# Performance work log

Hardware: AMD Instinct MI355X
Metric: run time of the kernel (lower is better)

## Reference

```python
import jax, jax.numpy as jnp
import numpy as np

HOPS = 2
BN_EPS = 1e-5


def _glorot(key, shape):
    fan_in = shape[-2]
    bound = 1.0 / np.sqrt(fan_in)
    return jax.random.uniform(key, shape, jnp.float32, -bound, bound)


def setup_inputs() -> dict:
    key = jax.random.key(0)
    ks = jax.random.split(key, 12)
    n, e = 50000, 800000
    in_c, hid, out_c = 128, 96, 64
    x = jax.random.normal(ks[0], (n, in_c), jnp.float32)
    edge_index = jax.random.randint(ks[1], (2, e), 0, n, jnp.int32)
    # MixHopLayer 0: hops+1 linears in_c -> hid (stacked)
    conv0_W = _glorot(ks[2], (HOPS + 1, in_c, hid))
    conv0_b = jnp.zeros((HOPS + 1, hid), jnp.float32)
    # MixHopLayer 1: hops+1 linears hid*(hops+1) -> out_c
    conv1_W = _glorot(ks[3], (HOPS + 1, hid * (HOPS + 1), out_c))
    conv1_b = jnp.zeros((HOPS + 1, out_c), jnp.float32)
    # BatchNorm1d(hid*(hops+1)) eval-mode params/buffers
    w = hid * (HOPS + 1)
    bn_gamma = jnp.ones((w,), jnp.float32)
    bn_beta = jnp.zeros((w,), jnp.float32)
    bn_mean = 0.1 * jax.random.normal(ks[4], (w,), jnp.float32)
    bn_var = jnp.ones((w,), jnp.float32) + 0.1 * jax.random.uniform(ks[5], (w,))
    # final projection out_c*(hops+1) -> out_c
    fp_W = _glorot(ks[6], (out_c * (HOPS + 1), out_c))
    fp_b = jnp.zeros((out_c,), jnp.float32)
    return dict(x=x, edge_index=edge_index, conv0_W=conv0_W, conv0_b=conv0_b,
                conv1_W=conv1_W, conv1_b=conv1_b, bn_gamma=bn_gamma, bn_beta=bn_beta,
                bn_mean=bn_mean, bn_var=bn_var, fp_W=fp_W, fp_b=fp_b)


def _gcn_norm(edge_index, n):
    # PyG gcn_norm with add_self_loops=True, improved=False, symmetric norm.
    row, col = edge_index[0], edge_index[1]
    loop = jnp.arange(n, dtype=edge_index.dtype)
    row = jnp.concatenate([row, loop])
    col = jnp.concatenate([col, loop])
    deg = jax.ops.segment_sum(jnp.ones_like(col, jnp.float32), col, num_segments=n)
    dinv = jnp.where(deg > 0, jax.lax.rsqrt(deg), 0.0)
    w = dinv[row] * dinv[col]
    return row, col, w


def _spmm_adj_t(row, col, w, x, n):
    # adj_t = SparseTensor(row=col, col=row, value=w): out[col] += w * x[row]
    return jax.ops.segment_sum(w[:, None] * x[row], col, num_segments=n)


def _mixhop_layer(x, W, b, row, col, w, n):
    xs = [x @ W[0] + b[0]]
    for j in range(1, HOPS + 1):
        xj = x @ W[j] + b[j]
        for _ in range(j):
            xj = _spmm_adj_t(row, col, w, xj, n)
        xs.append(xj)
    return jnp.concatenate(xs, axis=1)


def reference(x, edge_index, conv0_W, conv0_b, conv1_W, conv1_b,
              bn_gamma, bn_beta, bn_mean, bn_var, fp_W, fp_b):
    n = x.shape[0]
    row, col, w = _gcn_norm(edge_index, n)
    h = _mixhop_layer(x, conv0_W, conv0_b, row, col, w, n)
    # BatchNorm1d (eval) + ReLU; dropout is identity in eval
    h = bn_gamma * (h - bn_mean) * jax.lax.rsqrt(bn_var + BN_EPS) + bn_beta
    h = jax.nn.relu(h)
    h = _mixhop_layer(h, conv1_W, conv1_b, row, col, w, n)
    return h @ fp_W + fp_b
```

## Files before the change

kernel.cpp:

```cpp
#include <hip/hip_runtime.h>

#define IN_C 128
#define HID 96
#define OUT_C 64
#define W0C 288
#define W1C 192
#define CAP 5120
#define EPB 1024

typedef __bf16 bf16x8v __attribute__((ext_vector_type(8)));
typedef float  f32x4v  __attribute__((ext_vector_type(4)));


__global__ void k_combo_prep(const float* __restrict__ x, __bf16* __restrict__ xb, int n8,
                             const float* __restrict__ W0, const float* __restrict__ W1,
                             const float* __restrict__ Wf,
                             const float* __restrict__ gamma, const float* __restrict__ beta,
                             const float* __restrict__ mean, const float* __restrict__ var,
                             __bf16* __restrict__ w0t, __bf16* __restrict__ w1t,
                             __bf16* __restrict__ wft,
                             float* __restrict__ scale, float* __restrict__ shift,
                             int* __restrict__ zp, int nz,
                             int CB, int PB) {
    int b = blockIdx.x;
    if (b < CB) {
        int i = b * 256 + threadIdx.x;
        if (i >= n8) return;
        bf16x8v o;
#pragma unroll
        for (int q = 0; q < 8; q++) o[q] = (__bf16)x[i * 8 + q];
        *(bf16x8v*)(xb + (size_t)i * 8) = o;
    } else if (b < CB + PB) {
        const int T0 = 3 * IN_C * HID;
        const int T1 = 3 * W0C * OUT_C;
        const int T2 = W1C * OUT_C;
        int i = (b - CB) * 256 + threadIdx.x;
        if (i < T0) {
            int kn = IN_C * HID;
            int j = i / kn, r = i % kn;
            int k = r / HID, nn = r % HID;
            w0t[(size_t)j * kn + (size_t)nn * IN_C + k] = (__bf16)W0[i];
        } else if (i < T0 + T1) {
            int ii = i - T0;
            int kn = W0C * OUT_C;
            int j = ii / kn, r = ii % kn;
            int k = r / OUT_C, nn = r % OUT_C;
            w1t[(size_t)j * kn + (size_t)nn * W0C + k] = (__bf16)W1[ii];
        } else if (i < T0 + T1 + T2) {
            int ii = i - T0 - T1;
            int k = ii / OUT_C, nn = ii % OUT_C;
            wft[(size_t)nn * W1C + k] = (__bf16)Wf[ii];
        } else if (i < T0 + T1 + T2 + W0C) {
            int ii = i - T0 - T1 - T2;
            float s = gamma[ii] * rsqrtf(var[ii] + 1e-5f);
            scale[ii] = s;
            shift[ii] = beta[ii] - mean[ii] * s;
        }
    } else {
        int i = (b - CB - PB) * 256 + threadIdx.x;
        if (i < nz) zp[i] = 0;
    }
}

__global__ __launch_bounds__(256) void k_mega0(
        const int* __restrict__ row, const int* __restrict__ col,
        int* __restrict__ bcur ,
        int* __restrict__ binned, int e, int SB,
        const __bf16* __restrict__ xb, const __bf16* __restrict__ w0t ,
        const float* __restrict__ bias , __bf16* __restrict__ h,
        const float* __restrict__ scale, const float* __restrict__ shift, int M) {
    const int RS = 104;
    __shared__ __bf16 tile[128 * RS];
    int tid = threadIdx.x;
    if ((int)blockIdx.x < SB) {
        int* hist  = (int*)tile;
        int* basep = hist + 256;
        int e0 = blockIdx.x * EPB;
        int cnt = min(EPB, e - e0);
        hist[tid] = 0;
        __syncthreads();
        int rr[4], cc[4], rk[4];
#pragma unroll
        for (int k = 0; k < 4; k++) {
            int idx = tid + k * 256;
            if (idx < cnt) {
                rr[k] = row[e0 + idx];
                cc[k] = col[e0 + idx];
                rk[k] = atomicAdd(&hist[cc[k] >> 8], 1);
            }
        }
        __syncthreads();
        {
            int hv = hist[tid];
            if (hv > 0) basep[tid] = atomicAdd(&bcur[tid * 16], hv);
        }
        __syncthreads();
#pragma unroll
        for (int k = 0; k < 4; k++) {
            int idx = tid + k * 256;
            if (idx < cnt) {
                int b = cc[k] >> 8;
                int pos = basep[b] + rk[k];
                if (pos < CAP)
                    binned[(size_t)b * CAP + pos] = (rr[k] << 8) | (cc[k] & 255);
            }
        }
        return;
    }
    int wave = tid >> 6, lane = tid & 63;
    int ln = lane & 15, quad = lane >> 4;
    int rowBase = (blockIdx.x - SB) * 128;
    int waveRow = wave * 16;
    f32x4v acc[2][6];
#pragma unroll
    for (int u = 0; u < 2; u++)
#pragma unroll
        for (int t = 0; t < 6; t++) acc[u][t] = (f32x4v){0.f, 0.f, 0.f, 0.f};
    const __bf16* arow0 = xb + (size_t)(rowBase + waveRow + ln) * IN_C + quad * 8;
    const __bf16* arow1 = arow0 + (size_t)64 * IN_C;
#pragma unroll
    for (int k = 0; k < 4; k++) {
        bf16x8v a0 = *(const bf16x8v*)(arow0 + k * 32);
        bf16x8v a1 = *(const bf16x8v*)(arow1 + k * 32);
#pragma unroll
        for (int c = 0; c < 6; c++) {
            bf16x8v b = *(const bf16x8v*)(w0t + (size_t)(c * 16 + ln) * IN_C + k * 32 + quad * 8);
            acc[0][c] = __builtin_amdgcn_mfma_f32_16x16x32_bf16(a0, b, acc[0][c], 0, 0, 0);
            acc[1][c] = __builtin_amdgcn_mfma_f32_16x16x32_bf16(a1, b, acc[1][c], 0, 0, 0);
        }
    }
#pragma unroll
    for (int u = 0; u < 2; u++)
#pragma unroll
        for (int r = 0; r < 4; r++) {
            int lr = u * 64 + waveRow + quad * 4 + r;
#pragma unroll
            for (int c = 0; c < 6; c++) {
                int col2 = c * 16 + ln;
                float v = acc[u][c][r] + bias[col2];
                v = fmaxf(v * scale[col2] + shift[col2], 0.f);
                tile[lr * RS + col2] = (__bf16)v;
            }
        }
    __syncthreads();
#pragma unroll
    for (int s = 0; s < 6; s++) {
        int idx = tid + s * 256;
        int r = idx / 12, c8 = idx % 12;
        int grow = rowBase + r;
        if (grow < M)
            *(bf16x8v*)(h + (size_t)grow * W0C + c8 * 8) =
                *(const bf16x8v*)(tile + r * RS + c8 * 8);
    }
}

__global__ __launch_bounds__(256) void k_bucket_all(
        const int* __restrict__ binned, const int* __restrict__ bcur,
        float* __restrict__ dinv, int* __restrict__ csrs, int* __restrict__ row_ptr,
        int n, int nb) {
    __shared__ int s_pack[CAP];
    __shared__ int s_ofs[256];
    __shared__ int lcur[256];
    __shared__ int s_scan[256];
    int tid = threadIdx.x;
    int b = blockIdx.x;
    int node0 = b << 8;
    int v = (tid < nb) ? bcur[tid * 16] : 0;
    s_scan[tid] = v;
    __syncthreads();
    for (int o = 1; o < 256; o <<= 1) {
        int u = (tid >= o) ? s_scan[tid - o] : 0;
        __syncthreads();
        s_scan[tid] += u;
        __syncthreads();
    }
    int base = (b > 0) ? s_scan[b - 1] : 0;
    int cnt = min(bcur[b * 16], CAP);
    const int* bin = binned + (size_t)b * CAP;
    s_scan[tid] = 0;
    lcur[tid] = 0;
    __syncthreads();
    for (int t = tid; t < cnt; t += 256) {
        int p = bin[t];
        atomicAdd(&s_scan[p & 255], 1);
        atomicAdd(&lcur[p >> 16], 1);
    }
    __syncthreads();
    int cdeg = s_scan[tid];
    int node = node0 + tid;
    if (node < n) dinv[node] = rsqrtf((float)(cdeg + 1));
    s_ofs[tid] = cdeg;
    __syncthreads();
    for (int o = 1; o < 256; o <<= 1) {
        int u = (tid >= o) ? s_ofs[tid - o] : 0;
        __syncthreads();
        s_ofs[tid] += u;
        __syncthreads();
    }
    int nodeOfs = s_ofs[tid] - cdeg;
    if (node < n) {
        row_ptr[node] = base + nodeOfs;
        if (node == n - 1) row_ptr[n] = base + nodeOfs + cdeg;
    }
    __syncthreads();
    {
        int vv = lcur[tid];
        s_ofs[tid] = vv;
        __syncthreads();
        for (int o = 1; o < 256; o <<= 1) {
            int u = (tid >= o) ? s_ofs[tid - o] : 0;
            __syncthreads();
            s_ofs[tid] += u;
            __syncthreads();
        }
        lcur[tid] = s_ofs[tid] - vv;
    }
    __syncthreads();
    for (int t = tid; t < cnt; t += 256) {
        int p = bin[t];
        int pos = atomicAdd(&lcur[p >> 16], 1);
        s_pack[pos] = p;
    }
    __syncthreads();
    s_ofs[tid] = nodeOfs;
    lcur[tid] = 0;
    __syncthreads();
    for (int t = tid; t < cnt; t += 256) {
        int p = s_pack[t];
        int r = p >> 8;
        int local = p & 255;
        int pos = s_ofs[local] + atomicAdd(&lcur[local], 1);
        csrs[base + pos] = r;
    }
}


__global__ __launch_bounds__(256) void k_mf_l0b(
        const __bf16* __restrict__ s1, const __bf16* __restrict__ w0t,
        const float* __restrict__ bias , const float* __restrict__ arow,
        __bf16* __restrict__ h, __bf16* __restrict__ tp,
        const float* __restrict__ scale, const float* __restrict__ shift, int M) {
    const int RS = 104;
    __shared__ __bf16 tile[64 * RS];
    int tid = threadIdx.x;
    int wave = tid >> 6, lane = tid & 63;
    int ln = lane & 15, quad = lane >> 4;
    int rowBase = blockIdx.x * 64;
    int waveRow = wave * 16;
    const __bf16* w1p = w0t + (size_t)1 * HID * IN_C;
    const __bf16* w2p = w0t + (size_t)2 * HID * IN_C;
    f32x4v acc[2][6];
#pragma unroll
    for (int j = 0; j < 2; j++)
#pragma unroll
        for (int t = 0; t < 6; t++) acc[j][t] = (f32x4v){0.f, 0.f, 0.f, 0.f};
    const __bf16* arow0 = s1 + (size_t)(rowBase + waveRow + ln) * IN_C + quad * 8;
#pragma unroll
    for (int k = 0; k < 4; k++) {
        bf16x8v a0 = *(const bf16x8v*)(arow0 + k * 32);
#pragma unroll
        for (int c = 0; c < 6; c++) {
            bf16x8v b1 = *(const bf16x8v*)(w1p + (size_t)(c * 16 + ln) * IN_C + k * 32 + quad * 8);
            bf16x8v b2 = *(const bf16x8v*)(w2p + (size_t)(c * 16 + ln) * IN_C + k * 32 + quad * 8);
            acc[0][c] = __builtin_amdgcn_mfma_f32_16x16x32_bf16(a0, b1, acc[0][c], 0, 0, 0);
            acc[1][c] = __builtin_amdgcn_mfma_f32_16x16x32_bf16(a0, b2, acc[1][c], 0, 0, 0);
        }
    }
    float avs[4];
#pragma unroll
    for (int r = 0; r < 4; r++)
        avs[r] = arow[rowBase + waveRow + quad * 4 + r];
#pragma unroll
    for (int jj = 0; jj < 2; jj++) {
        const float* bj = bias + (jj + 1) * HID;
#pragma unroll
        for (int r = 0; r < 4; r++) {
            int lr = waveRow + quad * 4 + r;
            float av = avs[r];
#pragma unroll
            for (int c = 0; c < 6; c++) {
                int col = c * 16 + ln;
                float v = acc[jj][c][r] + av * bj[col];
                if (jj == 0) v = fmaxf(v * scale[HID + col] + shift[HID + col], 0.f);
                tile[lr * RS + col] = (__bf16)v;
            }
        }
        __syncthreads();
#pragma unroll
        for (int s = 0; s < 3; s++) {
            int idx = tid + s * 256;
            int r = idx / 12, c8 = idx % 12;
            int grow = rowBase + r;
            if (grow < M) {
                __bf16* dst = (jj == 0) ? (h + (size_t)grow * W0C + HID)
                                        : (tp + (size_t)grow * HID);
                *(bf16x8v*)(dst + c8 * 8) = *(const bf16x8v*)(tile + r * RS + c8 * 8);
            }
        }
        __syncthreads();
    }
}

__global__ __launch_bounds__(256) void k_mf_l1pf(
        const __bf16* __restrict__ hb, const __bf16* __restrict__ w1t ,
        const float* __restrict__ bias ,
        const __bf16* __restrict__ wft , const float* __restrict__ bf,
        __bf16* __restrict__ p0b, __bf16* __restrict__ p1b, __bf16* __restrict__ p2b,
        int M) {
    const int RS = 72;
    __shared__ __bf16 tile[64 * RS];
    int tid = threadIdx.x;
    int wave = tid >> 6, lane = tid & 63;
    int ln = lane & 15, quad = lane >> 4;
    int rowBase = blockIdx.x * 64;
    int waveRow = wave * 16;
    f32x4v acc[3][4];
#pragma unroll
    for (int j = 0; j < 3; j++)
#pragma unroll
        for (int t = 0; t < 4; t++) acc[j][t] = (f32x4v){0.f, 0.f, 0.f, 0.f};
    const __bf16* arow0 = hb + (size_t)(rowBase + waveRow + ln) * W0C + quad * 8;
#pragma unroll
    for (int k = 0; k < 9; k++) {
        bf16x8v a0 = *(const bf16x8v*)(arow0 + k * 32);
#pragma unroll
        for (int c = 0; c < 4; c++) {
#pragma unroll
            for (int j = 0; j < 3; j++) {
                bf16x8v b = *(const bf16x8v*)(w1t + (size_t)j * OUT_C * W0C +
                                              (size_t)(c * 16 + ln) * W0C + k * 32 + quad * 8);
                acc[j][c] = __builtin_amdgcn_mfma_f32_16x16x32_bf16(a0, b, acc[j][c], 0, 0, 0);
            }
        }
    }
#pragma unroll
    for (int j = 0; j < 3; j++) {
        const float* bj = bias + j * OUT_C;
#pragma unroll
        for (int r = 0; r < 4; r++) {
            int lr = waveRow + quad * 4 + r;
#pragma unroll
            for (int c = 0; c < 4; c++) {
                int col = c * 16 + ln;
                tile[lr * RS + col] = (__bf16)(acc[j][c][r] + bj[col]);
            }
        }
        f32x4v acc2[4];
#pragma unroll
        for (int t = 0; t < 4; t++) acc2[t] = (f32x4v){0.f, 0.f, 0.f, 0.f};
#pragma unroll
        for (int kk = 0; kk < 2; kk++) {
            bf16x8v a = *(const bf16x8v*)(tile + (waveRow + ln) * RS + kk * 32 + quad * 8);
#pragma unroll
            for (int c = 0; c < 4; c++) {
                bf16x8v b = *(const bf16x8v*)(wft + (size_t)(c * 16 + ln) * W1C +
                                              j * 64 + kk * 32 + quad * 8);
                acc2[c] = __builtin_amdgcn_mfma_f32_16x16x32_bf16(a, b, acc2[c], 0, 0, 0);
            }
        }
#pragma unroll
        for (int r = 0; r < 4; r++) {
            int lr = waveRow + quad * 4 + r;
#pragma unroll
            for (int c = 0; c < 4; c++) {
                int col = c * 16 + ln;
                float v = acc2[c][r] + (j == 0 ? bf[col] : 0.f);
                tile[lr * RS + col] = (__bf16)v;
            }
        }
        __syncthreads();
        __bf16* dst = (j == 0) ? p0b : ((j == 1) ? p1b : p2b);
#pragma unroll
        for (int s = 0; s < 2; s++) {
            int idx = tid + s * 256;
            int r = idx / 8, c8 = idx % 8;
            int grow = rowBase + r;
            if (grow < M)
                *(bf16x8v*)(dst + (size_t)grow * 64 + c8 * 8) =
                    *(const bf16x8v*)(tile + r * RS + c8 * 8);
        }
        __syncthreads();
    }
}

template <int C8, int NPB, bool BNRELU, bool AROW, bool ADDIN>
__global__ void k_spmm(const __bf16* __restrict__ xin, int ldx,
                       __bf16* __restrict__ xout, int ldo,
                       const int* __restrict__ row_ptr,
                       const int* __restrict__ csrs,
                       const float* __restrict__ dinv, int n,
                       const float* __restrict__ scale, const float* __restrict__ shift,
                       int chan0, float* __restrict__ arow,
                       const __bf16* __restrict__ addin) {
    int c8 = threadIdx.x % C8;
    int nl = threadIdx.x / C8;
    int node = blockIdx.x * NPB + nl;
    if (node >= n) return;
    float di = dinv[node];
    float lw = di * di;
    float acc[8];
    {
        bf16x8v v = *(const bf16x8v*)(xin + (size_t)node * ldx + c8 * 8);
#pragma unroll
        for (int q = 0; q < 8; q++) acc[q] = lw * (float)v[q];
    }
    float aw = lw;
    int start = row_ptr[node];
    int cnt = row_ptr[node + 1] - start;
    const int* cp = csrs + start;
    int k = 0;
    for (; k + 4 <= cnt; k += 4) {
        int s0 = cp[k + 0], s1 = cp[k + 1], s2 = cp[k + 2], s3 = cp[k + 3];
        float w0 = dinv[s0] * di, w1 = dinv[s1] * di;
        float w2 = dinv[s2] * di, w3 = dinv[s3] * di;
        bf16x8v v0 = *(const bf16x8v*)(xin + (size_t)s0 * ldx + c8 * 8);
        bf16x8v v1 = *(const bf16x8v*)(xin + (size_t)s1 * ldx + c8 * 8);
        bf16x8v v2 = *(const bf16x8v*)(xin + (size_t)s2 * ldx + c8 * 8);
        bf16x8v v3 = *(const bf16x8v*)(xin + (size_t)s3 * ldx + c8 * 8);
#pragma unroll
        for (int q = 0; q < 8; q++)
            acc[q] += w0 * (float)v0[q] + w1 * (float)v1[q] +
                      w2 * (float)v2[q] + w3 * (float)v3[q];
        if (AROW) aw += w0 + w1 + w2 + w3;
    }
    for (; k < cnt; k++) {
        int s = cp[k];
        float w = dinv[s] * di;
        bf16x8v xv = *(const bf16x8v*)(xin + (size_t)s * ldx + c8 * 8);
#pragma unroll
        for (int q = 0; q < 8; q++) acc[q] += w * (float)xv[q];
        if (AROW) aw += w;
    }
    if (AROW && c8 == 0) arow[node] = aw;
    bf16x8v ai;
    if (ADDIN) ai = *(const bf16x8v*)(addin + (size_t)node * 64 + c8 * 8);
    bf16x8v o;
#pragma unroll
    for (int q = 0; q < 8; q++) {
        float v = acc[q];
        if (ADDIN) v += (float)ai[q];
        if (BNRELU) {
            int ch = chan0 + c8 * 8 + q;
            v = fmaxf(v * scale[ch] + shift[ch], 0.f);
        }
        o[q] = (__bf16)v;
    }
    *(bf16x8v*)(xout + (size_t)node * ldo + c8 * 8) = o;
}

__global__ void k_spmm_fin(const __bf16* __restrict__ qin ,
                           const __bf16* __restrict__ p0b ,
                           const int* __restrict__ row_ptr, const int* __restrict__ csrs,
                           const float* __restrict__ dinv, int n,
                           float* __restrict__ out) {
    int c8 = threadIdx.x % 8;
    int nl = threadIdx.x / 8;
    int node = blockIdx.x * 32 + nl;
    if (node >= n) return;
    float di = dinv[node];
    float lw = di * di;
    float acc[8];
    {
        bf16x8v v = *(const bf16x8v*)(qin + (size_t)node * 64 + c8 * 8);
#pragma unroll
        for (int q = 0; q < 8; q++) acc[q] = lw * (float)v[q];
    }
    int start = row_ptr[node];
    int cnt = row_ptr[node + 1] - start;
    const int* cp = csrs + start;
    int k = 0;
    for (; k + 4 <= cnt; k += 4) {
        int s0 = cp[k + 0], s1 = cp[k + 1], s2 = cp[k + 2], s3 = cp[k + 3];
        float w0 = dinv[s0] * di, w1 = dinv[s1] * di;
        float w2 = dinv[s2] * di, w3 = dinv[s3] * di;
        bf16x8v v0 = *(const bf16x8v*)(qin + (size_t)s0 * 64 + c8 * 8);
        bf16x8v v1 = *(const bf16x8v*)(qin + (size_t)s1 * 64 + c8 * 8);
        bf16x8v v2 = *(const bf16x8v*)(qin + (size_t)s2 * 64 + c8 * 8);
        bf16x8v v3 = *(const bf16x8v*)(qin + (size_t)s3 * 64 + c8 * 8);
#pragma unroll
        for (int q = 0; q < 8; q++)
            acc[q] += w0 * (float)v0[q] + w1 * (float)v1[q] +
                      w2 * (float)v2[q] + w3 * (float)v3[q];
    }
    for (; k < cnt; k++) {
        int s = cp[k];
        float w = dinv[s] * di;
        bf16x8v xv = *(const bf16x8v*)(qin + (size_t)s * 64 + c8 * 8);
#pragma unroll
        for (int q = 0; q < 8; q++) acc[q] += w * (float)xv[q];
    }
    bf16x8v pv = *(const bf16x8v*)(p0b + (size_t)node * 64 + c8 * 8);
    f32x4v o0, o1;
#pragma unroll
    for (int q = 0; q < 4; q++) o0[q] = acc[q] + (float)pv[q];
#pragma unroll
    for (int q = 0; q < 4; q++) o1[q] = acc[4 + q] + (float)pv[4 + q];
    *(f32x4v*)(out + (size_t)node * OUT_C + c8 * 8) = o0;
    *(f32x4v*)(out + (size_t)node * OUT_C + c8 * 8 + 4) = o1;
}


extern "C" void kernel_launch(void* const* d_in, const int* in_sizes, int n_in,
                              void* d_out, int out_size, void* d_ws, size_t ws_size,
                              hipStream_t stream) {
    const int n = in_sizes[0] / IN_C;
    const int e = in_sizes[1] / 2;

    const float* x    = (const float*)d_in[0];
    const int*   ei   = (const int*)d_in[1];
    const float* W0   = (const float*)d_in[2];
    const float* b0   = (const float*)d_in[3];
    const float* W1   = (const float*)d_in[4];
    const float* b1   = (const float*)d_in[5];
    const float* bn_g = (const float*)d_in[6];
    const float* bn_b = (const float*)d_in[7];
    const float* bn_m = (const float*)d_in[8];
    const float* bn_v = (const float*)d_in[9];
    const float* Wf   = (const float*)d_in[10];
    const float* bf   = (const float*)d_in[11];
    float* out = (float*)d_out;

    const int* e_row = ei;
    const int* e_col = ei + e;

    char* ws = (char*)d_ws;
    size_t off = 0;
    auto alloc = [&](size_t bytes) -> void* {
        void* p = ws + off;
        off += (bytes + 255) & ~(size_t)255;
        return p;
    };
    const int NP = n + 128;
    int nb = (n + 255) / 256;

    int*    bcur    = (int*)alloc((size_t)256 * 16 * 4);
    int*    row_ptr = (int*)alloc((size_t)(n + 1) * 4);
    float*  dinv    = (float*)alloc((size_t)n * 4);
    float*  arow    = (float*)alloc((size_t)NP * 4);
    int*    binned  = (int*)alloc((size_t)nb * CAP * 4);
    int*    csrs    = (int*)alloc((size_t)e * 4);
    float*  bnscale = (float*)alloc(W0C * 4);
    float*  bnshift = (float*)alloc(W0C * 4);
    __bf16* xb  = (__bf16*)alloc((size_t)NP * IN_C * 2);
    __bf16* w0t = (__bf16*)alloc((size_t)3 * HID * IN_C * 2);
    __bf16* w1t = (__bf16*)alloc((size_t)3 * OUT_C * W0C * 2);
    __bf16* wft = (__bf16*)alloc((size_t)OUT_C * W1C * 2);
    __bf16* s1  = (__bf16*)alloc((size_t)NP * 128 * 2);
    __bf16* tp  = (__bf16*)alloc((size_t)NP * HID * 2);
    __bf16* h   = (__bf16*)alloc((size_t)NP * W0C * 2);
    __bf16* p0b = (__bf16*)alloc((size_t)NP * OUT_C * 2);
    __bf16* p1b = (__bf16*)alloc((size_t)NP * OUT_C * 2);
    __bf16* p2b = (__bf16*)alloc((size_t)NP * OUT_C * 2);
    __bf16* qb  = tp;

    int n8 = n * IN_C / 8;
    int nz = 256 * 16;
    int ptotal = 3 * IN_C * HID + 3 * W0C * OUT_C + W1C * OUT_C + W0C;
    int CB = (n8 + 255) / 256;
    int PB = (ptotal + 255) / 256;
    int ZB = (nz + 255) / 256;
    k_combo_prep<<<dim3(CB + PB + ZB), dim3(256), 0, stream>>>(
        x, xb, n8, W0, W1, Wf, bn_g, bn_b, bn_m, bn_v,
        w0t, w1t, wft, bnscale, bnshift, bcur, nz, CB, PB);

    int SB = (e + EPB - 1) / EPB;
    int GG = (n + 127) / 128;
    k_mega0<<<dim3(SB + GG), dim3(256), 0, stream>>>(
        e_row, e_col, bcur, binned, e, SB,
        xb, w0t, b0, h, bnscale, bnshift, n);

    k_bucket_all<<<dim3(nb), dim3(256), 0, stream>>>(binned, bcur, dinv, csrs,
                                                     row_ptr, n, nb);

    dim3 g64((n + 63) / 64);

    k_spmm<16, 16, false, true, false><<<dim3((n + 15) / 16), dim3(256), 0, stream>>>(
        xb, IN_C, s1, 128, row_ptr, csrs, dinv, n, nullptr, nullptr, 0, arow, nullptr);
    k_mf_l0b<<<g64, dim3(256), 0, stream>>>(s1, w0t, b0, arow, h, tp, bnscale, bnshift, n);
    k_spmm<12, 16, true, false, false><<<dim3((n + 15) / 16), dim3(192), 0, stream>>>(
        tp, HID, h + 2 * HID, W0C, row_ptr, csrs, dinv, n, bnscale, bnshift,
        2 * HID, nullptr, nullptr);

    k_mf_l1pf<<<g64, dim3(256), 0, stream>>>(h, w1t, b1, wft, bf, p0b, p1b, p2b, n);

    k_spmm<8, 32, false, false, true><<<dim3((n + 31) / 32), dim3(256), 0, stream>>>(
        p2b, OUT_C, qb, OUT_C, row_ptr, csrs, dinv, n, nullptr, nullptr, 0,
        nullptr, p1b);
    k_spmm_fin<<<dim3((n + 31) / 32), dim3(256), 0, stream>>>(
        qb, p0b, row_ptr, csrs, dinv, n, out);
}
```

Baseline: 304.1 us.

## Split layer-1 fused GEMM across blockIdx.y and stage weight tiles in LDS

The layer-1 MFMA kernel now runs one of the three hop linears per block via blockIdx.y, tripling the grid and cutting accumulator registers from 12 to 4 tiles. Each k-step's weight slice is cooperatively loaded into shared memory and read from there instead of every wave fetching it from global memory. The cost is reading the A rows three times from global memory and adding two barriers per k-step.

Result: faster. 290.9 us (-4.3%).

```diff
diff --git a/kernel.cpp b/kernel.cpp
--- a/kernel.cpp
+++ b/kernel.cpp
@@ -308,33 +308,36 @@
         __bf16* __restrict__ p0b, __bf16* __restrict__ p1b, __bf16* __restrict__ p2b,
         int M) {
     const int RS = 72;
+    const int BS = 40;
     __shared__ __bf16 tile[64 * RS];
+    __shared__ __bf16 bst[64 * BS];
     int tid = threadIdx.x;
     int wave = tid >> 6, lane = tid & 63;
     int ln = lane & 15, quad = lane >> 4;
+    int j = blockIdx.y;
     int rowBase = blockIdx.x * 64;
     int waveRow = wave * 16;
-    f32x4v acc[3][4];
-#pragma unroll
-    for (int j = 0; j < 3; j++)
-#pragma unroll
-        for (int t = 0; t < 4; t++) acc[j][t] = (f32x4v){0.f, 0.f, 0.f, 0.f};
+    f32x4v acc[4];
+#pragma unroll
+    for (int t = 0; t < 4; t++) acc[t] = (f32x4v){0.f, 0.f, 0.f, 0.f};
     const __bf16* arow0 = hb + (size_t)(rowBase + waveRow + ln) * W0C + quad * 8;
-#pragma unroll
+    int sr = tid >> 2, sseg = tid & 3;
+    const __bf16* bsrc = w1t + (size_t)j * OUT_C * W0C + (size_t)sr * W0C + sseg * 8;
+    __bf16* bdst = bst + (size_t)sr * BS + sseg * 8;
     for (int k = 0; k < 9; k++) {
+        bf16x8v tv = *(const bf16x8v*)(bsrc + k * 32);
         bf16x8v a0 = *(const bf16x8v*)(arow0 + k * 32);
+        __syncthreads();
+        *(bf16x8v*)bdst = tv;
+        __syncthreads();
 #pragma unroll
         for (int c = 0; c < 4; c++) {
-#pragma unroll
-            for (int j = 0; j < 3; j++) {
-                bf16x8v b = *(const bf16x8v*)(w1t + (size_t)j * OUT_C * W0C +
-                                              (size_t)(c * 16 + ln) * W0C + k * 32 + quad * 8);
-                acc[j][c] = __builtin_amdgcn_mfma_f32_16x16x32_bf16(a0, b, acc[j][c], 0, 0, 0);
-            }
-        }
-    }
-#pragma unroll
-    for (int j = 0; j < 3; j++) {
+            bf16x8v b = *(const bf16x8v*)(bst + (size_t)(c * 16 + ln) * BS + quad * 8);
+            acc[c] = __builtin_amdgcn_mfma_f32_16x16x32_bf16(a0, b, acc[c], 0, 0, 0);
+        }
+    }
+    __syncthreads();
+    {
         const float* bj = bias + j * OUT_C;
 #pragma unroll
         for (int r = 0; r < 4; r++) {
@@ -342,7 +345,7 @@
 #pragma unroll
             for (int c = 0; c < 4; c++) {
                 int col = c * 16 + ln;
-                tile[lr * RS + col] = (__bf16)(acc[j][c][r] + bj[col]);
+                tile[lr * RS + col] = (__bf16)(acc[c][r] + bj[col]);
             }
         }
         f32x4v acc2[4];
@@ -379,7 +382,6 @@
                 *(bf16x8v*)(dst + (size_t)grow * 64 + c8 * 8) =
                     *(const bf16x8v*)(tile + r * RS + c8 * 8);
         }
-        __syncthreads();
     }
 }
 
@@ -581,7 +583,8 @@
         tp, HID, h + 2 * HID, W0C, row_ptr, csrs, dinv, n, bnscale, bnshift,
         2 * HID, nullptr, nullptr);
 
-    k_mf_l1pf<<<g64, dim3(256), 0, stream>>>(h, w1t, b1, wft, bf, p0b, p1b, p2b, n);
+    k_mf_l1pf<<<dim3(g64.x, 3), dim3(256), 0, stream>>>(h, w1t, b1, wft, bf,
+                                                        p0b, p1b, p2b, n);
 
     k_spmm<8, 32, false, false, true><<<dim3((n + 31) / 32), dim3(256), 0, stream>>>(
         p2b, OUT_C, qb, OUT_C, row_ptr, csrs, dinv, n, nullptr, nullptr, 0,
```
